# Kernel optimization log

Measured on AMD Instinct MI355X. Metric: run time of the kernel, lower is better.

The kernel has to match this reference:

```python
import jax, jax.numpy as jnp
import numpy as np

EMBED = 1024
N_IMG, N_REG = 32, 36
N_CAP, MAX_W = 32, 32
EPS = 1e-8
LAMBDA_SM = 9.0
MARGIN = 0.2
ITER_STEPS = 3


def setup_inputs() -> dict:
    key = jax.random.key(0)
    k = jax.random.split(key, 8)
    img_emb = jax.random.normal(k[0], (N_IMG, N_REG, EMBED), dtype=jnp.float32)
    cap_emb = jax.random.normal(k[1], (N_CAP, MAX_W, EMBED), dtype=jnp.float32)
    cap_lens = jnp.maximum(jax.random.randint(k[2], (N_CAP,), 0, MAX_W + 1), 1)
    s = 1.0 / np.sqrt(2 * EMBED)
    w_lin = jax.random.uniform(k[3], (EMBED, 2 * EMBED), jnp.float32, -s, s)
    b_lin = jax.random.uniform(k[4], (EMBED,), jnp.float32, -s, s)
    w_gate = jax.random.uniform(k[5], (EMBED, 2 * EMBED), jnp.float32, -s, s)
    b_gate = jax.random.uniform(k[6], (EMBED,), jnp.float32, -s, s)
    return {"img_emb": img_emb, "cap_emb": cap_emb, "cap_lens": cap_lens,
            "w_lin": w_lin, "b_lin": b_lin, "w_gate": w_gate, "b_gate": b_gate}


def reference(img_emb, cap_emb, cap_lens, w_lin, b_lin, w_gate, b_gate):
    C, W, D = cap_emb.shape
    I, R, _ = img_emb.shape
    dt = cap_emb.dtype
    # word validity mask replaces the per-caption Python crop to n_word
    mask = (jnp.arange(W)[None, :] < cap_lens[:, None]).astype(dt)  # [C,W]
    cap_e = cap_emb[:, None]                     # [C,1,W,D] fixed query for cosine
    q = jnp.broadcast_to(cap_e, (C, I, W, D))    # evolving query per (cap,img)
    inv_len = 1.0 / cap_lens.astype(dt)          # [C]
    score = jnp.zeros((C, I), dt)
    for _ in range(ITER_STEPS):
        # raw attention: context(images) @ query^T -> [C,I,R,W]
        attn = jnp.einsum('ird,ciwd->cirw', img_emb, q)
        attn = jax.nn.leaky_relu(attn, 0.1)
        # clipped_l2norm over the (valid) word axis
        nrm = jnp.sqrt(jnp.sum(jnp.square(attn * mask[:, None, None, :]),
                               axis=3, keepdims=True)) + EPS
        attn = attn / nrm
        # smooth softmax over regions (per word)
        sm = jax.nn.softmax(attn * LAMBDA_SM, axis=2)
        wc = jnp.einsum('cirw,ird->ciwd', sm, img_emb)  # weighted context [C,I,W,D]
        # cosine similarity between original caption words and attended feats
        w12 = jnp.sum(cap_e * wc, axis=-1)                       # [C,I,W]
        w1 = jnp.sqrt(jnp.sum(jnp.square(cap_e), axis=-1))       # [C,1,W]
        w2 = jnp.sqrt(jnp.sum(jnp.square(wc), axis=-1))          # [C,I,W]
        cos = w12 / jnp.maximum(w1 * w2, EPS)
        score = score + jnp.sum(cos * mask[:, None, :], axis=2) * inv_len[:, None]
        # gated memory fusion (t2i)
        cat = jnp.concatenate([q, wc], axis=-1)                  # [C,I,W,2D]
        h = jnp.tanh(cat @ w_lin.T + b_lin)
        g = jax.nn.sigmoid(cat @ w_gate.T + b_gate)
        q = q * g + h * (1.0 - g)
    # score is [n_caption, n_image] (training-mode transpose in original)
    diag = jnp.diagonal(score)
    cost_s = jnp.clip(MARGIN + score - diag[:, None], 0.0)
    cost_im = jnp.clip(MARGIN + score - diag[None, :], 0.0)
    eye = jnp.eye(C, dtype=bool)
    cost_s = jnp.where(eye, 0.0, cost_s)
    cost_im = jnp.where(eye, 0.0, cost_im)
    return jnp.sum(jnp.max(cost_s, axis=1)) + jnp.sum(jnp.max(cost_im, axis=0))
```

## Files before the change

### kernel.cpp

```cpp
#include <hip/hip_runtime.h>
#include <hip/hip_fp16.h>

#define C_ 32
#define I_ 32
#define W_ 32
#define R_ 36
#define D_ 1024
#define EPS_ 1e-8f
#define LAMBDA_ 9.0f
#define MARGIN_ 0.2f

typedef _Float16 f16;
typedef f16 half8 __attribute__((ext_vector_type(8)));
typedef f16 f16x4 __attribute__((ext_vector_type(4)));
typedef float f32x4 __attribute__((ext_vector_type(4)));

__device__ __forceinline__ void gload16(const void* g, void* l) {
    __builtin_amdgcn_global_load_lds((const __attribute__((address_space(1))) void*)g,
                                     (__attribute__((address_space(3))) void*)l, 16, 0, 0);
}

__device__ __forceinline__ f16x4 to_h4(f32x4 v) {
    f16x4 o; o[0] = (f16)v[0]; o[1] = (f16)v[1]; o[2] = (f16)v[2]; o[3] = (f16)v[3];
    return o;
}

__global__ __launch_bounds__(256) void convert_kernel(
    const float* __restrict__ cap, const float* __restrict__ wl, const float* __restrict__ wg,
    const float* __restrict__ img,
    f16* __restrict__ capH, f16* __restrict__ wlH, f16* __restrict__ wgH, f16* __restrict__ imgH)
{
    const int t = blockIdx.x * 256 + threadIdx.x;
    const float* src; f16* dst; int idx;
    if (t < 262144)        { src = cap; dst = capH; idx = t; }
    else if (t < 786432)   { src = wl;  dst = wlH;  idx = t - 262144; }
    else if (t < 1310720)  { src = wg;  dst = wgH;  idx = t - 786432; }
    else                   { src = img; dst = imgH; idx = t - 1310720; }
    float4 v = ((const float4*)src)[idx];
    f16x4 o; o[0] = (f16)v.x; o[1] = (f16)v.y; o[2] = (f16)v.z; o[3] = (f16)v.w;
    *(f16x4*)(dst + (size_t)idx * 4) = o;
}

__global__ __launch_bounds__(64) void w11_kernel(const float* __restrict__ cap,
                                                 float* __restrict__ w11Buf,
                                                 const int* __restrict__ lens,
                                                 int* __restrict__ tileMap,
                                                 int* __restrict__ activeCnt)
{
    if (blockIdx.x == 0 && threadIdx.x == 63) {
        int n = 0;
        for (int cm = 0; cm < 256; cm++) {
            const int len = lens[cm >> 3];
            if ((cm & 7) * 4 < len) tileMap[n++] = cm;
        }
        activeCnt[0] = n;
    }
    const int row = blockIdx.x;
    const float* p = cap + (size_t)row * 1024;
    float s = 0.f;
    for (int e = threadIdx.x; e < 1024; e += 64) { float v = p[e]; s += v * v; }
    for (int off = 32; off > 0; off >>= 1) s += __shfl_down(s, off);
    if (threadIdx.x == 0) w11Buf[row] = s;
}

__global__ __launch_bounds__(256) void gram_kernel(const f16* __restrict__ imgH,
                                                   f16* __restrict__ gramH)
{
    __shared__ f16 sG[2][48 * 128];
    const int i = blockIdx.x;
    const int tid = threadIdx.x, lane = tid & 63, wv = tid >> 6;

    auto stage = [&](int b, int k0) {
        for (int g = wv; g < 12; g += 4) {
            const int row = g * 4 + (lane >> 4);
            gload16(imgH + (size_t)(i * 36 + row) * 1024 + k0 + (((lane & 15) ^ (row & 7)) << 3),
                    &sG[b][g * 512]);
        }
    };

    f32x4 acc[4];
    #pragma unroll
    for (int a = 0; a < 4; a++) acc[a] = (f32x4){0.f, 0.f, 0.f, 0.f};

    stage(0, 0);
    __syncthreads();
    int cur = 0;
    for (int kc = 0; kc < 8; kc++) {
        if (kc < 7) stage(cur ^ 1, (kc + 1) * 128);
        #pragma unroll
        for (int ks = 0; ks < 4; ks++) {
            const int arow = wv * 16 + (lane & 15);
            const half8 am = *(const half8*)&sG[cur][arow * 128 + ((((ks << 2) | (lane >> 4)) ^ (arow & 7)) << 3)];
            #pragma unroll
            for (int nt = 0; nt < 4; nt++) {
                const int brow = nt * 16 + (lane & 15);
                const half8 bn = *(const half8*)&sG[cur][brow * 128 + ((((ks << 2) | (lane >> 4)) ^ (brow & 7)) << 3)];
                acc[nt] = __builtin_amdgcn_mfma_f32_16x16x32_f16(am, bn, acc[nt], 0, 0, 0);
            }
        }
        __syncthreads();
        cur ^= 1;
    }
    #pragma unroll
    for (int nt = 0; nt < 4; nt++)
        #pragma unroll
        for (int r = 0; r < 4; r++) {
            const int m = wv * 16 + ((lane >> 4) << 2) + r;
            const int n = nt * 16 + (lane & 15);
            gramH[(size_t)i * 4096 + m * 64 + n] = (m < 36 && n < 36) ? (f16)acc[nt][r] : (f16)0.f;
        }
}

__global__ __launch_bounds__(256) void imgw2t_kernel(
    const f16* __restrict__ wlinH, const f16* __restrict__ wgateH,
    const f16* __restrict__ imgH, f16* __restrict__ imgW2T)
{
    const int jt = blockIdx.x;
    const int i  = blockIdx.y;
    __shared__ f16 sA[128 * 64];
    __shared__ f16 sB[64 * 64];
    const int tid = threadIdx.x, lane = tid & 63, wv = tid >> 6;
    const int wm = wv >> 1, wn = wv & 1;
    f32x4 acc[4][2];
    #pragma unroll
    for (int a = 0; a < 4; a++) { acc[a][0] = (f32x4){0,0,0,0}; acc[a][1] = (f32x4){0,0,0,0}; }

    for (int ks = 0; ks < 16; ks++) {
        const int kk = ks * 64;
        __syncthreads();
        #pragma unroll
        for (int p = 0; p < 4; p++) {
            const int u = tid + p * 256;
            const int row = u >> 3, ch = u & 7;
            const int jr = jt * 128 + row;
            const f16* src = ((jr < 1024) ? (wlinH + (size_t)jr * 2048)
                                          : (wgateH + (size_t)(jr - 1024) * 2048))
                             + 1024 + kk + ((ch ^ (row & 7)) << 3);
            gload16(src, (char*)sA + u * 16);
        }
        #pragma unroll
        for (int p = 0; p < 2; p++) {
            const int u = tid + p * 256;
            const int row = u >> 3, ch = u & 7;
            const f16* src = imgH + (size_t)(i * 36 + row) * 1024 + kk + ((ch ^ (row & 7)) << 3);
            gload16(src, (char*)sB + u * 16);
        }
        __syncthreads();
        #pragma unroll
        for (int ksub = 0; ksub < 2; ksub++) {
            const int kch = (ksub << 2) | (lane >> 4);
            half8 af[4], bf[2];
            #pragma unroll
            for (int tm = 0; tm < 4; tm++) {
                const int row = wm * 64 + tm * 16 + (lane & 15);
                af[tm] = *(const half8*)((const char*)sA + row * 128 + ((kch ^ (row & 7)) << 4));
            }
            #pragma unroll
            for (int tn = 0; tn < 2; tn++) {
                const int row = wn * 32 + tn * 16 + (lane & 15);
                bf[tn] = *(const half8*)((const char*)sB + row * 128 + ((kch ^ (row & 7)) << 4));
            }
            #pragma unroll
            for (int tm = 0; tm < 4; tm++)
                #pragma unroll
                for (int tn = 0; tn < 2; tn++)
                    acc[tm][tn] = __builtin_amdgcn_mfma_f32_16x16x32_f16(af[tm], bf[tn], acc[tm][tn], 0, 0, 0);
        }
    }
    #pragma unroll
    for (int tm = 0; tm < 4; tm++)
        #pragma unroll
        for (int tn = 0; tn < 2; tn++)
            #pragma unroll
            for (int r = 0; r < 4; r++) {
                const int j = jt * 128 + wm * 64 + tm * 16 + (lane >> 4) * 4 + r;
                const int rc = wn * 32 + tn * 16 + (lane & 15);
                imgW2T[((size_t)i * 2048 + j) * 64 + rc] = (rc < 36) ? (f16)acc[tm][tn][r] : (f16)0.f;
            }
}

__device__ __forceinline__ float smt_read(const f16* sSmT, int w, int r) {
    return (float)sSmT[w * 64 + ((((r >> 3) ^ (w & 7)) << 3) | (r & 7))];
}

template<int MODE>
__global__ __launch_bounds__(256, 3) void attn_kernel(
    const f16* __restrict__ imgH,
    const f16* __restrict__ gramH,
    const f16* __restrict__ imgW2T,
    const f16* __restrict__ capH,
    const f16* __restrict__ qcur,
    const f16* __restrict__ capW1,
    f16* __restrict__ capImg0,
    const float* __restrict__ b_lin, const float* __restrict__ b_gate,
    const float* __restrict__ w11Buf,
    const int* __restrict__ lens,
    f16* __restrict__ preLin, f16* __restrict__ preGate,
    f16* __restrict__ qOut,
    float* __restrict__ score)
{
    constexpr int SBIG = (MODE == 0) ? 33792 : 28672;
    __shared__ __align__(16) char sBig[SBIG];
    __shared__ f16 sSmT[2][2048];
    __shared__ float sAttn[36][66];
    __shared__ float sNrm[2][36];
    __shared__ float sW22[2][4][32];
    __shared__ float sW12f[2][32];

    const int bid = blockIdx.x;
    const int cp = bid >> 5;
    const int i  = ((bid & 7) << 2) | ((bid >> 3) & 3);
    const int c0 = cp * 2;
    const int len0 = lens[c0], len1 = lens[c0 + 1];
    const int tid = threadIdx.x;
    const int lane = tid & 63;
    const int wv = tid >> 6;
    const int i36 = i * 36;

    f16* sPA = (f16*)sBig;

    f32x4 accA[3] = {{0,0,0,0},{0,0,0,0},{0,0,0,0}};
    const int lenW = (wv >> 1) ? len1 : len0;
    const bool skipW = (MODE != 0) && ((wv & 1) == 1) && (lenW <= 16);

    auto stageA = [&](int k0) {
        for (int g = wv; g < 28; g += 4) {
            if (g < 12) {
                const int row = g * 4 + (lane >> 4);
                gload16(imgH + (size_t)(i36 + row) * 1024 + k0 + (((lane & 15) ^ (row & 7)) << 3),
                        &sPA[g * 512]);
            } else {
                const int gq = g - 12;
                const int w = gq * 4 + (lane >> 4);
                const int lenw = (w >> 5) ? len1 : len0;
                const f16* src = (MODE == 0)
                    ? (capH + (size_t)(c0 * 32 + w) * 1024)
                    : (qcur + (((size_t)(c0 * 32 + w)) * 32 + i) * 1024);
                src += k0 + (((lane & 15) ^ (w & 7)) << 3);
                if (MODE == 0 || (w & 31) < lenw)
                    gload16(src, &sPA[6144 + gq * 512]);
            }
        }
    };

    for (int kc = 0; kc < 8; kc++) {
        stageA(kc * 128);
        __syncthreads();
        if (!skipW) {
            __builtin_amdgcn_s_setprio(1);
            #pragma unroll
            for (int ks = 0; ks < 4; ks++) {
                const int kch = (ks << 2) | (lane >> 4);
                const int brow = wv * 16 + (lane & 15);
                const half8 bf = *(const half8*)&sPA[6144 + brow * 128 + ((kch ^ (brow & 7)) << 3)];
                #pragma unroll
                for (int mt = 0; mt < 3; mt++) {
                    const int arow = mt * 16 + (lane & 15);
                    const half8 af = *(const half8*)&sPA[arow * 128 + ((kch ^ (arow & 7)) << 3)];
                    accA[mt] = __builtin_amdgcn_mfma_f32_16x16x32_f16(af, bf, accA[mt], 0, 0, 0);
                }
            }
            __builtin_amdgcn_s_setprio(0);
        }
        __syncthreads();
    }

    if (!skipW) {
        #pragma unroll
        for (int mt = 0; mt < 3; mt++) {
            #pragma unroll
            for (int r = 0; r < 4; r++) {
                const int rr = mt * 16 + (lane >> 4) * 4 + r;
                if (rr < 36) {
                    float v = accA[mt][r];
                    sAttn[rr][wv * 16 + (lane & 15)] = (v >= 0.f) ? v : 0.1f * v;
                }
            }
        }
    }
    __syncthreads();

    if (tid < 72) {
        const int cap = tid / 36;
        const int r = tid - cap * 36;
        const int lenc = cap ? len1 : len0;
        float s = 0.f;
        for (int w = 0; w < lenc; w++) { float v = sAttn[r][cap * 32 + w]; s += v * v; }
        sNrm[cap][r] = LAMBDA_ / (sqrtf(s) + EPS_);
    }
    __syncthreads();

    if (tid < 64) {
        const int cap = tid >> 5, w = tid & 31;
        const int lenc = cap ? len1 : len0;
        f16* smt = &sSmT[cap][0];
        if (w < lenc) {
            float m = -1e30f;
            #pragma unroll
            for (int r = 0; r < 36; r++) m = fmaxf(m, sAttn[r][cap * 32 + w] * sNrm[cap][r]);
            float sum = 0.f;
            #pragma unroll
            for (int r = 0; r < 36; r++) sum += __expf(sAttn[r][cap * 32 + w] * sNrm[cap][r] - m);
            const float inv = 1.0f / sum;
            #pragma unroll
            for (int r = 0; r < 64; r++) {
                const int off = w * 64 + ((((r >> 3) ^ (w & 7)) << 3) | (r & 7));
                smt[off] = (r < 36) ? (f16)(__expf(sAttn[r][cap * 32 + w] * sNrm[cap][r] - m) * inv) : (f16)0.f;
            }
        } else {
            #pragma unroll
            for (int r = 0; r < 64; r++) smt[w * 64 + r] = (f16)0.f;
        }
    }
    __syncthreads();

    if (MODE == 0) {
        const int w = tid >> 3, rg = tid & 7;
        #pragma unroll
        for (int cap = 0; cap < 2; cap++) {
            half8 o;
            #pragma unroll
            for (int k = 0; k < 8; k++) {
                const int r = rg * 8 + k;
                float v = 0.f;
                if (r < 36) { v = sAttn[r][cap * 32 + w]; v = (v >= 0.f) ? v : v * 10.f; }
                o[k] = (f16)v;
            }
            const size_t base = ((((size_t)((c0 + cap) * 32 + i)) << 5) + w) << 6;
            *(half8*)(capImg0 + base + rg * 8) = o;
        }
    }

    half8 af[2][2][2];
    #pragma unroll
    for (int cap = 0; cap < 2; cap++)
        #pragma unroll
        for (int mt = 0; mt < 2; mt++)
            #pragma unroll
            for (int ks = 0; ks < 2; ks++) {
                const int row = mt * 16 + (lane & 15);
                af[cap][mt][ks] = *(const half8*)&sSmT[cap][row * 64 + ((((ks << 2) | (lane >> 4)) ^ (row & 7)) << 3)];
            }

    {
        const f16* gb = gramH + ((size_t)i << 12);
        const int arow = (wv << 4) + (lane & 15);
        const half8 gA0 = *(const half8*)(gb + arow * 64 + ((lane >> 4) << 3));
        const half8 gA1 = *(const half8*)(gb + arow * 64 + 32 + ((lane >> 4) << 3));
        float w22L[2][2] = {{0.f, 0.f}, {0.f, 0.f}};
        #pragma unroll
        for (int cap = 0; cap < 2; cap++)
            #pragma unroll
            for (int mt = 0; mt < 2; mt++) {
                f32x4 t = {0.f, 0.f, 0.f, 0.f};
                t = __builtin_amdgcn_mfma_f32_16x16x32_f16(gA0, af[cap][mt][0], t, 0, 0, 0);
                t = __builtin_amdgcn_mfma_f32_16x16x32_f16(gA1, af[cap][mt][1], t, 0, 0, 0);
                const int w = mt * 16 + (lane & 15);
                const int rp = (wv << 4) + ((lane >> 4) << 2);
                #pragma unroll
                for (int r = 0; r < 4; r++)
                    w22L[cap][mt] += t[r] * smt_read(&sSmT[cap][0], w, rp + r);
            }
        #pragma unroll
        for (int cap = 0; cap < 2; cap++)
            #pragma unroll
            for (int mt = 0; mt < 2; mt++) {
                w22L[cap][mt] += __shfl_xor(w22L[cap][mt], 16);
                w22L[cap][mt] += __shfl_xor(w22L[cap][mt], 32);
            }
        if (lane < 16) {
            #pragma unroll
            for (int cap = 0; cap < 2; cap++) {
                sW22[cap][wv][lane] = w22L[cap][0];
                sW22[cap][wv][16 + lane] = w22L[cap][1];
            }
        }
    }

    {
        const int w = tid >> 3, rg = tid & 7;
        #pragma unroll
        for (int cap = 0; cap < 2; cap++) {
            float p = 0.f;
            if (MODE == 0) {
                #pragma unroll
                for (int k = 0; k < 8; k++) {
                    const int r = rg * 8 + k;
                    if (r < 36) {
                        float v = sAttn[r][cap * 32 + w]; v = (v >= 0.f) ? v : v * 10.f;
                        p += v * smt_read(&sSmT[cap][0], w, r);
                    }
                }
            } else {
                const size_t base = ((((size_t)((c0 + cap) * 32 + i)) << 5) + w) << 6;
                const half8 ci8 = *(const half8*)(capImg0 + base + rg * 8);
                #pragma unroll
                for (int k = 0; k < 8; k++) {
                    const int r = rg * 8 + k;
                    if (r < 36) p += (float)ci8[k] * smt_read(&sSmT[cap][0], w, r);
                }
            }
            p += __shfl_xor(p, 1); p += __shfl_xor(p, 2); p += __shfl_xor(p, 4);
            if (rg == 0) sW12f[cap][w] = p;
        }
    }
    __syncthreads();

    if (tid < 64) {
        const int cap = tid >> 5, w = tid & 31;
        const int lenc = cap ? len1 : len0;
        float part = 0.f;
        if (w < lenc) {
            const float a = sW12f[cap][w];
            const float b = sW22[cap][0][w] + sW22[cap][1][w] + sW22[cap][2][w] + sW22[cap][3][w];
            part = a / fmaxf(sqrtf(w11Buf[(c0 + cap) * 32 + w]) * sqrtf(b), EPS_);
        }
        part += __shfl_down(part, 16);
        part += __shfl_down(part, 8);
        part += __shfl_down(part, 4);
        part += __shfl_down(part, 2);
        part += __shfl_down(part, 1);
        if ((lane & 31) == 0) score[(c0 + cap) * 32 + i] += part / (float)lenc;
    }

    if (MODE == 1) {
        f16 (*tiles)[2][32][66] = (f16(*)[2][32][66])sBig;
        const f16* w2base = imgW2T + (((size_t)i * 2048) << 6);
        half8 nb0, nb1;
        {
            const int jA = wv * 16 + (lane & 15);
            const f16* bb = w2base + ((size_t)jA << 6);
            nb0 = *(const half8*)(bb + ((lane >> 4) << 3));
            nb1 = *(const half8*)(bb + 32 + ((lane >> 4) << 3));
        }
        for (int t = 0; t < 32; t++) {
            const half8 bf0 = nb0, bf1 = nb1;
            if (t < 31) {
                const int jA = ((t + 1) * 4 + wv) * 16 + (lane & 15);
                const f16* bb = w2base + ((size_t)jA << 6);
                nb0 = *(const half8*)(bb + ((lane >> 4) << 3));
                nb1 = *(const half8*)(bb + 32 + ((lane >> 4) << 3));
            }
            __builtin_amdgcn_s_setprio(1);
            #pragma unroll
            for (int cap = 0; cap < 2; cap++)
                #pragma unroll
                for (int mt = 0; mt < 2; mt++) {
                    f32x4 acc = {0.f, 0.f, 0.f, 0.f};
                    acc = __builtin_amdgcn_mfma_f32_16x16x32_f16(bf0, af[cap][mt][0], acc, 0, 0, 0);
                    acc = __builtin_amdgcn_mfma_f32_16x16x32_f16(bf1, af[cap][mt][1], acc, 0, 0, 0);
                    const int w = mt * 16 + (lane & 15);
                    *(f16x4*)&tiles[t & 1][cap][w][wv * 16 + ((lane >> 4) << 2)] = to_h4(acc);
                }
            __builtin_amdgcn_s_setprio(0);
            __syncthreads();
            const int w = tid >> 3, jg = tid & 7;
            f16* dst = (t < 16) ? preLin : preGate;
            const int joff = ((t * 64) & 1023) + jg * 8;
            #pragma unroll
            for (int cap = 0; cap < 2; cap++) {
                const int lenc = cap ? len1 : len0;
                if (w < lenc) {
                    const half8 v = *(const half8*)&tiles[t & 1][cap][w][jg * 8];
                    *(half8*)(dst + (((size_t)((c0 + cap) * 32 + w) * 32 + i) << 10) + joff) = v;
                }
            }
        }
    } else if (MODE == 0) {
        f16 (*tiles)[2][2][32][66] = (f16(*)[2][2][32][66])sBig;
        const f16* w2base = imgW2T + (((size_t)i * 2048) << 6);
        half8 nL0, nL1, nG0, nG1;
        {
            const int jA = wv * 16 + (lane & 15);
            const f16* bbL = w2base + ((size_t)jA << 6);
            const f16* bbG = w2base + ((size_t)(1024 + jA) << 6);
            nL0 = *(const half8*)(bbL + ((lane >> 4) << 3));
            nL1 = *(const half8*)(bbL + 32 + ((lane >> 4) << 3));
            nG0 = *(const half8*)(bbG + ((lane >> 4) << 3));
            nG1 = *(const half8*)(bbG + 32 + ((lane >> 4) << 3));
        }
        for (int t = 0; t < 16; t++) {
            const half8 bL0 = nL0, bL1 = nL1, bG0 = nG0, bG1 = nG1;
            if (t < 15) {
                const int jA = ((t + 1) * 4 + wv) * 16 + (lane & 15);
                const f16* bbL = w2base + ((size_t)jA << 6);
                const f16* bbG = w2base + ((size_t)(1024 + jA) << 6);
                nL0 = *(const half8*)(bbL + ((lane >> 4) << 3));
                nL1 = *(const half8*)(bbL + 32 + ((lane >> 4) << 3));
                nG0 = *(const half8*)(bbG + ((lane >> 4) << 3));
                nG1 = *(const half8*)(bbG + 32 + ((lane >> 4) << 3));
            }
            __builtin_amdgcn_s_setprio(1);
            #pragma unroll
            for (int cap = 0; cap < 2; cap++)
                #pragma unroll
                for (int mt = 0; mt < 2; mt++) {
                    f32x4 aL = {0.f, 0.f, 0.f, 0.f}, aG = {0.f, 0.f, 0.f, 0.f};
                    aL = __builtin_amdgcn_mfma_f32_16x16x32_f16(bL0, af[cap][mt][0], aL, 0, 0, 0);
                    aL = __builtin_amdgcn_mfma_f32_16x16x32_f16(bL1, af[cap][mt][1], aL, 0, 0, 0);
                    aG = __builtin_amdgcn_mfma_f32_16x16x32_f16(bG0, af[cap][mt][0], aG, 0, 0, 0);
                    aG = __builtin_amdgcn_mfma_f32_16x16x32_f16(bG1, af[cap][mt][1], aG, 0, 0, 0);
                    const int w = mt * 16 + (lane & 15);
                    const int x = wv * 16 + ((lane >> 4) << 2);
                    *(f16x4*)&tiles[t & 1][cap][0][w][x] = to_h4(aL);
                    *(f16x4*)&tiles[t & 1][cap][1][w][x] = to_h4(aG);
                }
            __builtin_amdgcn_s_setprio(0);
            __syncthreads();
            const int w = tid >> 3, jg = tid & 7;
            const int j = t * 64 + jg * 8;
            #pragma unroll
            for (int cap = 0; cap < 2; cap++) {
                const int lenc = cap ? len1 : len0;
                if (w < lenc) {
                    const size_t cw = (size_t)((c0 + cap) * 32 + w);
                    const half8 l8 = *(const half8*)&tiles[t & 1][cap][0][w][jg * 8];
                    const half8 g8 = *(const half8*)&tiles[t & 1][cap][1][w][jg * 8];
                    const half8 c1L = *(const half8*)(capW1 + cw * 2048 + j);
                    const half8 c1G = *(const half8*)(capW1 + cw * 2048 + 1024 + j);
                    const half8 cp8 = *(const half8*)(capH + cw * 1024 + j);
                    half8 o;
                    #pragma unroll
                    for (int k = 0; k < 8; k++) {
                        const float h = tanhf((float)l8[k] + (float)c1L[k] + b_lin[j + k]);
                        const float g = 1.f / (1.f + __expf(-((float)g8[k] + (float)c1G[k] + b_gate[j + k])));
                        o[k] = (f16)((float)cp8[k] * g + h * (1.f - g));
                    }
                    *(half8*)(qOut + ((cw * 32 + i) << 10) + j) = o;
                }
            }
        }
    }
}

__global__ __launch_bounds__(256) void qgemm_kernel(
    const f16* __restrict__ Aptr,
    const f16* __restrict__ wlinH, const f16* __restrict__ wgateH,
    const f16* __restrict__ preLin, const f16* __restrict__ preGate,
    const float* __restrict__ b_lin, const float* __restrict__ b_gate,
    f16* __restrict__ outp,
    const int* __restrict__ lens,
    const int* __restrict__ tileMap, const int* __restrict__ activeCnt,
    const int mode)
{
    const int bid = blockIdx.x;
    int jt, cm;
    if (mode) {
        const int x = bid & 7;
        jt = (bid >> 3) & 15;
        const int s = bid >> 7;
        const int a = s * 8 + x;
        if (a >= activeCnt[0]) return;
        cm = tileMap[a];
    } else {
        jt = bid & 15; cm = bid >> 4;
    }
    int len = 32;
    if (mode) len = lens[cm >> 3];
    const int m0 = cm * 128;

    __shared__ f16 sA[128 * 64];
    __shared__ f16 sB[128 * 64];

    const int tid = threadIdx.x;
    const int lane = tid & 63;
    const int wv = tid >> 6;
    const int wm = wv >> 1;
    const int wn = wv & 1;

    f32x4 acc[4][4];
    #pragma unroll
    for (int a = 0; a < 4; a++)
        #pragma unroll
        for (int b = 0; b < 4; b++)
            acc[a][b] = (f32x4){0.f, 0.f, 0.f, 0.f};

    for (int ks = 0; ks < 16; ks++) {
        const int kk = ks * 64;
        #pragma unroll
        for (int p = 0; p < 4; p++) {
            const int idx = tid + p * 256;
            const int row = idx >> 3, ch = idx & 7;
            gload16(Aptr + (size_t)(m0 + row) * 1024 + kk + ((ch ^ (row & 7)) << 3),
                    (char*)sA + idx * 16);
        }
        #pragma unroll
        for (int p = 0; p < 4; p++) {
            const int idx = tid + p * 256;
            const int n = idx >> 3, ch = idx & 7;
            const int j = jt * 64 + (n & 63);
            const f16* wsrc = ((n < 64) ? wlinH : wgateH) + (size_t)j * 2048 + kk + ((ch ^ (n & 7)) << 3);
            gload16(wsrc, (char*)sB + idx * 16);
        }
        __syncthreads();
        #pragma unroll
        for (int ksub = 0; ksub < 2; ksub++) {
            const int k4 = (ksub << 2) | (lane >> 4);
            half8 afr[4], bfr[4];
            #pragma unroll
            for (int tm = 0; tm < 4; tm++) {
                const int row = wm * 64 + tm * 16 + (lane & 15);
                afr[tm] = *(const half8*)((const char*)sA + row * 128 + ((k4 ^ (row & 7)) << 4));
            }
            #pragma unroll
            for (int tn = 0; tn < 4; tn++) {
                const int n = wn * 64 + tn * 16 + (lane & 15);
                bfr[tn] = *(const half8*)((const char*)sB + n * 128 + ((k4 ^ (n & 7)) << 4));
            }
            #pragma unroll
            for (int tm = 0; tm < 4; tm++)
                #pragma unroll
                for (int tn = 0; tn < 4; tn++)
                    acc[tm][tn] = __builtin_amdgcn_mfma_f32_16x16x32_f16(afr[tm], bfr[tn], acc[tm][tn], 0, 0, 0);
        }
        __syncthreads();
    }

    f16 (*tl)[68] = (f16(*)[68])sA;
    f16 (*tg)[68] = (f16(*)[68])sB;
    const int j0 = (tid & 3) * 16;
    const int j = jt * 64 + j0;
    f32x4 blv[4], bgv[4];
    if (mode == 1) {
        #pragma unroll
        for (int q = 0; q < 4; q++) {
            blv[q] = *(const f32x4*)(b_lin + j + q * 4);
            bgv[q] = *(const f32x4*)(b_gate + j + q * 4);
        }
    }
    #pragma unroll
    for (int p = 0; p < 2; p++) {
        __syncthreads();
        if (wm == p) {
            #pragma unroll
            for (int tm = 0; tm < 4; tm++)
                #pragma unroll
                for (int tn = 0; tn < 4; tn++) {
                    const int n = wn * 64 + tn * 16 + (lane & 15);
                    #pragma unroll
                    for (int r = 0; r < 4; r++) {
                        const int ml = tm * 16 + ((lane >> 4) << 2) + r;
                        if (n < 64) tl[ml][n] = (f16)acc[tm][tn][r];
                        else        tg[ml][n - 64] = (f16)acc[tm][tn][r];
                    }
                }
        }
        __syncthreads();
        const int rl = tid >> 2;
        const int gm = m0 + p * 64 + rl;
        bool active = true;
        if (mode) active = (((gm >> 5) & 31) < len);
        if (active) {
            const half8 l0 = *(const half8*)&tl[rl][j0];
            const half8 l1 = *(const half8*)&tl[rl][j0 + 8];
            const half8 g0 = *(const half8*)&tg[rl][j0];
            const half8 g1 = *(const half8*)&tg[rl][j0 + 8];
            if (mode == 0) {
                *(half8*)(outp + (size_t)gm * 2048 + j) = l0;
                *(half8*)(outp + (size_t)gm * 2048 + j + 8) = l1;
                *(half8*)(outp + (size_t)gm * 2048 + 1024 + j) = g0;
                *(half8*)(outp + (size_t)gm * 2048 + 1024 + j + 8) = g1;
            } else {
                const size_t off = ((size_t)gm << 10) + j;
                const half8 pl0 = *(const half8*)(preLin + off);
                const half8 pl1 = *(const half8*)(preLin + off + 8);
                const half8 pg0 = *(const half8*)(preGate + off);
                const half8 pg1 = *(const half8*)(preGate + off + 8);
                const half8 qo0 = *(const half8*)(Aptr + off);
                const half8 qo1 = *(const half8*)(Aptr + off + 8);
                half8 o0, o1;
                #pragma unroll
                for (int k = 0; k < 8; k++) {
                    const float h = tanhf((float)l0[k] + (float)pl0[k] + blv[k >> 2][k & 3]);
                    const float g = 1.f / (1.f + __expf(-((float)g0[k] + (float)pg0[k] + bgv[k >> 2][k & 3])));
                    o0[k] = (f16)((float)qo0[k] * g + h * (1.f - g));
                }
                #pragma unroll
                for (int k = 0; k < 8; k++) {
                    const float h = tanhf((float)l1[k] + (float)pl1[k] + blv[2 + (k >> 2)][k & 3]);
                    const float g = 1.f / (1.f + __expf(-((float)g1[k] + (float)pg1[k] + bgv[2 + (k >> 2)][k & 3])));
                    o1[k] = (f16)((float)qo1[k] * g + h * (1.f - g));
                }
                *(half8*)(outp + off) = o0;
                *(half8*)(outp + off + 8) = o1;
            }
        }
    }
}

__global__ __launch_bounds__(64) void loss_kernel(const float* __restrict__ score,
                                                  float* __restrict__ out)
{
    __shared__ float s[32][33];
    __shared__ float diag[32];
    const int tid = threadIdx.x;
    for (int idx = tid; idx < 1024; idx += 64) s[idx >> 5][idx & 31] = score[idx];
    __syncthreads();
    if (tid < 32) diag[tid] = s[tid][tid];
    __syncthreads();
    float total = 0.f;
    if (tid < 32) {
        float m1 = 0.f, m2 = 0.f;
        for (int k = 0; k < 32; k++) {
            if (k != tid) {
                m1 = fmaxf(m1, fmaxf(0.f, MARGIN_ + s[tid][k] - diag[tid]));
                m2 = fmaxf(m2, fmaxf(0.f, MARGIN_ + s[k][tid] - diag[tid]));
            }
        }
        total = m1 + m2;
    }
    for (int off = 32; off > 0; off >>= 1) total += __shfl_down(total, off);
    if (tid == 0) out[0] = total;
}

extern "C" void kernel_launch(void* const* d_in, const int* in_sizes, int n_in,
                              void* d_out, int out_size, void* d_ws, size_t ws_size,
                              hipStream_t stream) {
    const float* img    = (const float*)d_in[0];
    const float* cap    = (const float*)d_in[1];
    const int*   lens   = (const int*)d_in[2];
    const float* w_lin  = (const float*)d_in[3];
    const float* b_lin  = (const float*)d_in[4];
    const float* w_gate = (const float*)d_in[5];
    const float* b_gate = (const float*)d_in[6];
    float* out = (float*)d_out;

    char* ws = (char*)d_ws;
    f16* qA      = (f16*)(ws);
    f16* preLin  = (f16*)(ws + 67108864);
    f16* preGate = (f16*)(ws + 134217728);
    f16* capH    = (f16*)(ws + 201326592);
    f16* wlinH   = (f16*)(ws + 203423744);
    f16* wgateH  = (f16*)(ws + 207618048);
    f16* imgH    = (f16*)(ws + 211812352);
    f16* gramH   = (f16*)(ws + 214958080);
    f16* capImg0 = (f16*)(ws + 216006656);
    f16* imgW2T  = (f16*)(ws + 220200960);
    f16* capW1   = (f16*)(ws + 228589568);
    float* w11Buf = (float*)(ws + 232783872);
    float* score  = (float*)(ws + 232787968);
    int* tileMap  = (int*)(ws + 232792064);
    int* activeCnt= (int*)(ws + 232793088);
    f16* qB = preLin;

    hipMemsetAsync(score, 0, C_ * I_ * sizeof(float), stream);
    convert_kernel<<<dim3(6272), dim3(256), 0, stream>>>(cap, w_lin, w_gate, img, capH, wlinH, wgateH, imgH);
    w11_kernel<<<dim3(1024), dim3(64), 0, stream>>>(cap, w11Buf, lens, tileMap, activeCnt);
    gram_kernel<<<dim3(32), dim3(256), 0, stream>>>(imgH, gramH);
    imgw2t_kernel<<<dim3(16, 32), dim3(256), 0, stream>>>(wlinH, wgateH, imgH, imgW2T);
    qgemm_kernel<<<dim3(128), dim3(256), 0, stream>>>(capH, wlinH, wgateH, (const f16*)0, (const f16*)0,
                                                      b_lin, b_gate, capW1, lens, tileMap, activeCnt, 0);
    attn_kernel<0><<<dim3(512), dim3(256), 0, stream>>>(imgH, gramH, imgW2T, capH, (const f16*)0,
                                                        capW1, capImg0, b_lin, b_gate, w11Buf, lens,
                                                        preLin, preGate, qA, score);
    attn_kernel<1><<<dim3(512), dim3(256), 0, stream>>>(imgH, gramH, imgW2T, capH, qA,
                                                        capW1, capImg0, b_lin, b_gate, w11Buf, lens,
                                                        preLin, preGate, (f16*)0, score);
    qgemm_kernel<<<dim3(2432), dim3(256), 0, stream>>>(qA, wlinH, wgateH, preLin, preGate,
                                                       b_lin, b_gate, qB, lens, tileMap, activeCnt, 1);
    attn_kernel<2><<<dim3(512), dim3(256), 0, stream>>>(imgH, gramH, imgW2T, capH, qB,
                                                        capW1, capImg0, b_lin, b_gate, w11Buf, lens,
                                                        preLin, preGate, (f16*)0, score);

    loss_kernel<<<dim3(1), dim3(64), 0, stream>>>(score, out);
}
```

Before: 407.7 us.

## Merge gram and imgW2T prep kernels; process two j-subtiles per iteration in mode 1

The gram and image-times-weight precompute kernels become one launch with 544 blocks: the first 512 compute imgW2T and the last 32 compute the Gram matrix. This removes one launch and lets the small gram work overlap the larger GEMM. Separately, the MODE 1 attention path now computes two 64-column subtiles per loop iteration (16 iterations instead of 32), halving the barriers and grouping more MFMAs per step. In exchange it needs a larger shared tile buffer in MODE 1, which may lower occupancy.

```diff
diff --git a/kernel.cpp b/kernel.cpp
--- a/kernel.cpp
+++ b/kernel.cpp
@@ -63,120 +63,119 @@
     if (threadIdx.x == 0) w11Buf[row] = s;
 }
 
-__global__ __launch_bounds__(256) void gram_kernel(const f16* __restrict__ imgH,
-                                                   f16* __restrict__ gramH)
+__global__ __launch_bounds__(256) void imgprep_kernel(
+    const f16* __restrict__ wlinH, const f16* __restrict__ wgateH,
+    const f16* __restrict__ imgH, f16* __restrict__ imgW2T, f16* __restrict__ gramH)
 {
-    __shared__ f16 sG[2][48 * 128];
-    const int i = blockIdx.x;
+    __shared__ __align__(16) char sMem[24576];
     const int tid = threadIdx.x, lane = tid & 63, wv = tid >> 6;
 
-    auto stage = [&](int b, int k0) {
-        for (int g = wv; g < 12; g += 4) {
-            const int row = g * 4 + (lane >> 4);
-            gload16(imgH + (size_t)(i * 36 + row) * 1024 + k0 + (((lane & 15) ^ (row & 7)) << 3),
-                    &sG[b][g * 512]);
-        }
-    };
-
-    f32x4 acc[4];
-    #pragma unroll
-    for (int a = 0; a < 4; a++) acc[a] = (f32x4){0.f, 0.f, 0.f, 0.f};
-
-    stage(0, 0);
-    __syncthreads();
-    int cur = 0;
-    for (int kc = 0; kc < 8; kc++) {
-        if (kc < 7) stage(cur ^ 1, (kc + 1) * 128);
-        #pragma unroll
-        for (int ks = 0; ks < 4; ks++) {
-            const int arow = wv * 16 + (lane & 15);
-            const half8 am = *(const half8*)&sG[cur][arow * 128 + ((((ks << 2) | (lane >> 4)) ^ (arow & 7)) << 3)];
-            #pragma unroll
-            for (int nt = 0; nt < 4; nt++) {
-                const int brow = nt * 16 + (lane & 15);
-                const half8 bn = *(const half8*)&sG[cur][brow * 128 + ((((ks << 2) | (lane >> 4)) ^ (brow & 7)) << 3)];
-                acc[nt] = __builtin_amdgcn_mfma_f32_16x16x32_f16(am, bn, acc[nt], 0, 0, 0);
-            }
-        }
+    if (blockIdx.x < 512) {
+        const int jt = blockIdx.x & 15;
+        const int i  = blockIdx.x >> 4;
+        f16* sA = (f16*)sMem;
+        f16* sB = (f16*)(sMem + 16384);
+        const int wm = wv >> 1, wn = wv & 1;
+        f32x4 acc[4][2];
+        #pragma unroll
+        for (int a = 0; a < 4; a++) { acc[a][0] = (f32x4){0,0,0,0}; acc[a][1] = (f32x4){0,0,0,0}; }
+
+        for (int ks = 0; ks < 16; ks++) {
+            const int kk = ks * 64;
+            __syncthreads();
+            #pragma unroll
+            for (int p = 0; p < 4; p++) {
+                const int u = tid + p * 256;
+                const int row = u >> 3, ch = u & 7;
+                const int jr = jt * 128 + row;
+                const f16* src = ((jr < 1024) ? (wlinH + (size_t)jr * 2048)
+                                              : (wgateH + (size_t)(jr - 1024) * 2048))
+                                 + 1024 + kk + ((ch ^ (row & 7)) << 3);
+                gload16(src, (char*)sA + u * 16);
+            }
+            #pragma unroll
+            for (int p = 0; p < 2; p++) {
+                const int u = tid + p * 256;
+                const int row = u >> 3, ch = u & 7;
+                const f16* src = imgH + (size_t)(i * 36 + row) * 1024 + kk + ((ch ^ (row & 7)) << 3);
+                gload16(src, (char*)sB + u * 16);
+            }
+            __syncthreads();
+            #pragma unroll
+            for (int ksub = 0; ksub < 2; ksub++) {
+                const int kch = (ksub << 2) | (lane >> 4);
+                half8 af[4], bf[2];
+                #pragma unroll
+                for (int tm = 0; tm < 4; tm++) {
+                    const int row = wm * 64 + tm * 16 + (lane & 15);
+                    af[tm] = *(const half8*)((const char*)sA + row * 128 + ((kch ^ (row & 7)) << 4));
+                }
+                #pragma unroll
+                for (int tn = 0; tn < 2; tn++) {
+                    const int row = wn * 32 + tn * 16 + (lane & 15);
+                    bf[tn] = *(const half8*)((const char*)sB + row * 128 + ((kch ^ (row & 7)) << 4));
+                }
+                #pragma unroll
+                for (int tm = 0; tm < 4; tm++)
+                    #pragma unroll
+                    for (int tn = 0; tn < 2; tn++)
+                        acc[tm][tn] = __builtin_amdgcn_mfma_f32_16x16x32_f16(af[tm], bf[tn], acc[tm][tn], 0, 0, 0);
+            }
+        }
+        #pragma unroll
+        for (int tm = 0; tm < 4; tm++)
+            #pragma unroll
+            for (int tn = 0; tn < 2; tn++)
+                #pragma unroll
+                for (int r = 0; r < 4; r++) {
+                    const int j = jt * 128 + wm * 64 + tm * 16 + (lane >> 4) * 4 + r;
+                    const int rc = wn * 32 + tn * 16 + (lane & 15);
+                    imgW2T[((size_t)i * 2048 + j) * 64 + rc] = (rc < 36) ? (f16)acc[tm][tn][r] : (f16)0.f;
+                }
+    } else {
+        const int i = blockIdx.x - 512;
+        f16 (*sG)[6144] = (f16(*)[6144])sMem;
+
+        auto stage = [&](int b, int k0) {
+            for (int g = wv; g < 12; g += 4) {
+                const int row = g * 4 + (lane >> 4);
+                gload16(imgH + (size_t)(i * 36 + row) * 1024 + k0 + (((lane & 15) ^ (row & 7)) << 3),
+                        &sG[b][g * 512]);
+            }
+        };
+
+        f32x4 acc[4];
+        #pragma unroll
+        for (int a = 0; a < 4; a++) acc[a] = (f32x4){0.f, 0.f, 0.f, 0.f};
+
+        stage(0, 0);
         __syncthreads();
-        cur ^= 1;
-    }
-    #pragma unroll
-    for (int nt = 0; nt < 4; nt++)
-        #pragma unroll
-        for (int r = 0; r < 4; r++) {
-            const int m = wv * 16 + ((lane >> 4) << 2) + r;
-            const int n = nt * 16 + (lane & 15);
-            gramH[(size_t)i * 4096 + m * 64 + n] = (m < 36 && n < 36) ? (f16)acc[nt][r] : (f16)0.f;
-        }
-}
-
-__global__ __launch_bounds__(256) void imgw2t_kernel(
-    const f16* __restrict__ wlinH, const f16* __restrict__ wgateH,
-    const f16* __restrict__ imgH, f16* __restrict__ imgW2T)
-{
-    const int jt = blockIdx.x;
-    const int i  = blockIdx.y;
-    __shared__ f16 sA[128 * 64];
-    __shared__ f16 sB[64 * 64];
-    const int tid = threadIdx.x, lane = tid & 63, wv = tid >> 6;
-    const int wm = wv >> 1, wn = wv & 1;
-    f32x4 acc[4][2];
-    #pragma unroll
-    for (int a = 0; a < 4; a++) { acc[a][0] = (f32x4){0,0,0,0}; acc[a][1] = (f32x4){0,0,0,0}; }
-
-    for (int ks = 0; ks < 16; ks++) {
-        const int kk = ks * 64;
-        __syncthreads();
-        #pragma unroll
-        for (int p = 0; p < 4; p++) {
-            const int u = tid + p * 256;
-            const int row = u >> 3, ch = u & 7;
-            const int jr = jt * 128 + row;
-            const f16* src = ((jr < 1024) ? (wlinH + (size_t)jr * 2048)
-                                          : (wgateH + (size_t)(jr - 1024) * 2048))
-                             + 1024 + kk + ((ch ^ (row & 7)) << 3);
-            gload16(src, (char*)sA + u * 16);
-        }
-        #pragma unroll
-        for (int p = 0; p < 2; p++) {
-            const int u = tid + p * 256;
-            const int row = u >> 3, ch = u & 7;
-            const f16* src = imgH + (size_t)(i * 36 + row) * 1024 + kk + ((ch ^ (row & 7)) << 3);
-            gload16(src, (char*)sB + u * 16);
-        }
-        __syncthreads();
-        #pragma unroll
-        for (int ksub = 0; ksub < 2; ksub++) {
-            const int kch = (ksub << 2) | (lane >> 4);
-            half8 af[4], bf[2];
-            #pragma unroll
-            for (int tm = 0; tm < 4; tm++) {
-                const int row = wm * 64 + tm * 16 + (lane & 15);
-                af[tm] = *(const half8*)((const char*)sA + row * 128 + ((kch ^ (row & 7)) << 4));
-            }
-            #pragma unroll
-            for (int tn = 0; tn < 2; tn++) {
-                const int row = wn * 32 + tn * 16 + (lane & 15);
-                bf[tn] = *(const half8*)((const char*)sB + row * 128 + ((kch ^ (row & 7)) << 4));
-            }
-            #pragma unroll
-            for (int tm = 0; tm < 4; tm++)
-                #pragma unroll
-                for (int tn = 0; tn < 2; tn++)
-                    acc[tm][tn] = __builtin_amdgcn_mfma_f32_16x16x32_f16(af[tm], bf[tn], acc[tm][tn], 0, 0, 0);
-        }
-    }
-    #pragma unroll
-    for (int tm = 0; tm < 4; tm++)
-        #pragma unroll
-        for (int tn = 0; tn < 2; tn++)
+        int cur = 0;
+        for (int kc = 0; kc < 8; kc++) {
+            if (kc < 7) stage(cur ^ 1, (kc + 1) * 128);
+            #pragma unroll
+            for (int ks = 0; ks < 4; ks++) {
+                const int arow = wv * 16 + (lane & 15);
+                const half8 am = *(const half8*)&sG[cur][arow * 128 + ((((ks << 2) | (lane >> 4)) ^ (arow & 7)) << 3)];
+                #pragma unroll
+                for (int nt = 0; nt < 4; nt++) {
+                    const int brow = nt * 16 + (lane & 15);
+                    const half8 bn = *(const half8*)&sG[cur][brow * 128 + ((((ks << 2) | (lane >> 4)) ^ (brow & 7)) << 3)];
+                    acc[nt] = __builtin_amdgcn_mfma_f32_16x16x32_f16(am, bn, acc[nt], 0, 0, 0);
+                }
+            }
+            __syncthreads();
+            cur ^= 1;
+        }
+        #pragma unroll
+        for (int nt = 0; nt < 4; nt++)
             #pragma unroll
             for (int r = 0; r < 4; r++) {
-                const int j = jt * 128 + wm * 64 + tm * 16 + (lane >> 4) * 4 + r;
-                const int rc = wn * 32 + tn * 16 + (lane & 15);
-                imgW2T[((size_t)i * 2048 + j) * 64 + rc] = (rc < 36) ? (f16)acc[tm][tn][r] : (f16)0.f;
-            }
+                const int m = wv * 16 + ((lane >> 4) << 2) + r;
+                const int n = nt * 16 + (lane & 15);
+                gramH[(size_t)i * 4096 + m * 64 + n] = (m < 36 && n < 36) ? (f16)acc[nt][r] : (f16)0.f;
+            }
+    }
 }
 
 __device__ __forceinline__ float smt_read(const f16* sSmT, int w, int r) {
@@ -199,7 +198,7 @@
     f16* __restrict__ qOut,
     float* __restrict__ score)
 {
-    constexpr int SBIG = (MODE == 0) ? 33792 : 28672;
+    constexpr int SBIG = (MODE == 2) ? 28672 : 33792;
     __shared__ __align__(16) char sBig[SBIG];
     __shared__ f16 sSmT[2][2048];
     __shared__ float sAttn[36][66];
@@ -424,50 +423,65 @@
     }
 
     if (MODE == 1) {
-        f16 (*tiles)[2][32][66] = (f16(*)[2][32][66])sBig;
+        f16 (*tiles)[4][32][66] = (f16(*)[4][32][66])sBig;
         const f16* w2base = imgW2T + (((size_t)i * 2048) << 6);
-        half8 nb0, nb1;
+        half8 nb[2][2];
         {
-            const int jA = wv * 16 + (lane & 15);
-            const f16* bb = w2base + ((size_t)jA << 6);
-            nb0 = *(const half8*)(bb + ((lane >> 4) << 3));
-            nb1 = *(const half8*)(bb + 32 + ((lane >> 4) << 3));
-        }
-        for (int t = 0; t < 32; t++) {
-            const half8 bf0 = nb0, bf1 = nb1;
-            if (t < 31) {
-                const int jA = ((t + 1) * 4 + wv) * 16 + (lane & 15);
+            #pragma unroll
+            for (int s = 0; s < 2; s++) {
+                const int jA = (s * 4 + wv) * 16 + (lane & 15);
                 const f16* bb = w2base + ((size_t)jA << 6);
-                nb0 = *(const half8*)(bb + ((lane >> 4) << 3));
-                nb1 = *(const half8*)(bb + 32 + ((lane >> 4) << 3));
+                nb[s][0] = *(const half8*)(bb + ((lane >> 4) << 3));
+                nb[s][1] = *(const half8*)(bb + 32 + ((lane >> 4) << 3));
+            }
+        }
+        for (int t = 0; t < 16; t++) {
+            half8 bf[2][2];
+            #pragma unroll
+            for (int s = 0; s < 2; s++) { bf[s][0] = nb[s][0]; bf[s][1] = nb[s][1]; }
+            if (t < 15) {
+                #pragma unroll
+                for (int s = 0; s < 2; s++) {
+                    const int sub = (t + 1) * 2 + s;
+                    const int jA = (sub * 4 + wv) * 16 + (lane & 15);
+                    const f16* bb = w2base + ((size_t)jA << 6);
+                    nb[s][0] = *(const half8*)(bb + ((lane >> 4) << 3));
+                    nb[s][1] = *(const half8*)(bb + 32 + ((lane >> 4) << 3));
+                }
             }
             __builtin_amdgcn_s_setprio(1);
             #pragma unroll
-            for (int cap = 0; cap < 2; cap++)
-                #pragma unroll
-                for (int mt = 0; mt < 2; mt++) {
-                    f32x4 acc = {0.f, 0.f, 0.f, 0.f};
-                    acc = __builtin_amdgcn_mfma_f32_16x16x32_f16(bf0, af[cap][mt][0], acc, 0, 0, 0);
-                    acc = __builtin_amdgcn_mfma_f32_16x16x32_f16(bf1, af[cap][mt][1], acc, 0, 0, 0);
-                    const int w = mt * 16 + (lane & 15);
-                    *(f16x4*)&tiles[t & 1][cap][w][wv * 16 + ((lane >> 4) << 2)] = to_h4(acc);
-                }
+            for (int s = 0; s < 2; s++)
+                #pragma unroll
+                for (int cap = 0; cap < 2; cap++)
+                    #pragma unroll
+                    for (int mt = 0; mt < 2; mt++) {
+                        f32x4 acc = {0.f, 0.f, 0.f, 0.f};
+                        acc = __builtin_amdgcn_mfma_f32_16x16x32_f16(bf[s][0], af[cap][mt][0], acc, 0, 0, 0);
+                        acc = __builtin_amdgcn_mfma_f32_16x16x32_f16(bf[s][1], af[cap][mt][1], acc, 0, 0, 0);
+                        const int w = mt * 16 + (lane & 15);
+                        *(f16x4*)&tiles[t & 1][cap * 2 + s][w][wv * 16 + ((lane >> 4) << 2)] = to_h4(acc);
+                    }
             __builtin_amdgcn_s_setprio(0);
             __syncthreads();
             const int w = tid >> 3, jg = tid & 7;
-            f16* dst = (t < 16) ? preLin : preGate;
-            const int joff = ((t * 64) & 1023) + jg * 8;
-            #pragma unroll
-            for (int cap = 0; cap < 2; cap++) {
-                const int lenc = cap ? len1 : len0;
-                if (w < lenc) {
-                    const half8 v = *(const half8*)&tiles[t & 1][cap][w][jg * 8];
-                    *(half8*)(dst + (((size_t)((c0 + cap) * 32 + w) * 32 + i) << 10) + joff) = v;
+            #pragma unroll
+            for (int s = 0; s < 2; s++) {
+                const int sub = t * 2 + s;
+                f16* dst = (sub < 16) ? preLin : preGate;
+                const int joff = ((sub * 64) & 1023) + jg * 8;
+                #pragma unroll
+                for (int cap = 0; cap < 2; cap++) {
+                    const int lenc = cap ? len1 : len0;
+                    if (w < lenc) {
+                        const half8 v = *(const half8*)&tiles[t & 1][cap * 2 + s][w][jg * 8];
+                        *(half8*)(dst + (((size_t)((c0 + cap) * 32 + w) * 32 + i) << 10) + joff) = v;
+                    }
                 }
             }
         }
     } else if (MODE == 0) {
-        f16 (*tiles)[2][2][32][66] = (f16(*)[2][2][32][66])sBig;
+        f16 (*tiles)[4][32][66] = (f16(*)[4][32][66])sBig;
         const f16* w2base = imgW2T + (((size_t)i * 2048) << 6);
         half8 nL0, nL1, nG0, nG1;
         {
@@ -502,8 +516,8 @@
                     aG = __builtin_amdgcn_mfma_f32_16x16x32_f16(bG1, af[cap][mt][1], aG, 0, 0, 0);
                     const int w = mt * 16 + (lane & 15);
                     const int x = wv * 16 + ((lane >> 4) << 2);
-                    *(f16x4*)&tiles[t & 1][cap][0][w][x] = to_h4(aL);
-                    *(f16x4*)&tiles[t & 1][cap][1][w][x] = to_h4(aG);
+                    *(f16x4*)&tiles[t & 1][cap * 2 + 0][w][x] = to_h4(aL);
+                    *(f16x4*)&tiles[t & 1][cap * 2 + 1][w][x] = to_h4(aG);
                 }
             __builtin_amdgcn_s_setprio(0);
             __syncthreads();
@@ -514,8 +528,8 @@
                 const int lenc = cap ? len1 : len0;
                 if (w < lenc) {
                     const size_t cw = (size_t)((c0 + cap) * 32 + w);
-                    const half8 l8 = *(const half8*)&tiles[t & 1][cap][0][w][jg * 8];
-                    const half8 g8 = *(const half8*)&tiles[t & 1][cap][1][w][jg * 8];
+                    const half8 l8 = *(const half8*)&tiles[t & 1][cap * 2 + 0][w][jg * 8];
+                    const half8 g8 = *(const half8*)&tiles[t & 1][cap * 2 + 1][w][jg * 8];
                     const half8 c1L = *(const half8*)(capW1 + cw * 2048 + j);
                     const half8 c1G = *(const half8*)(capW1 + cw * 2048 + 1024 + j);
                     const half8 cp8 = *(const half8*)(capH + cw * 1024 + j);
@@ -746,8 +760,7 @@
     hipMemsetAsync(score, 0, C_ * I_ * sizeof(float), stream);
     convert_kernel<<<dim3(6272), dim3(256), 0, stream>>>(cap, w_lin, w_gate, img, capH, wlinH, wgateH, imgH);
     w11_kernel<<<dim3(1024), dim3(64), 0, stream>>>(cap, w11Buf, lens, tileMap, activeCnt);
-    gram_kernel<<<dim3(32), dim3(256), 0, stream>>>(imgH, gramH);
-    imgw2t_kernel<<<dim3(16, 32), dim3(256), 0, stream>>>(wlinH, wgateH, imgH, imgW2T);
+    imgprep_kernel<<<dim3(544), dim3(256), 0, stream>>>(wlinH, wgateH, imgH, imgW2T, gramH);
     qgemm_kernel<<<dim3(128), dim3(256), 0, stream>>>(capH, wlinH, wgateH, (const f16*)0, (const f16*)0,
                                                       b_lin, b_gate, capW1, lens, tileMap, activeCnt, 0);
     attn_kernel<0><<<dim3(512), dim3(256), 0, stream>>>(imgH, gramH, imgW2T, capH, (const f16*)0,
```

Measured after the change: 399.7 us. About the same (-2.0%).
